# Kernel tuning notes

Measured on AMD Instinct MI355X. Metric: run time of the kernel, lower is better.

## Reference

```python
import jax, jax.numpy as jnp
import numpy as np

B, H, T, D = 2, 16, 2048, 64
BASE_WINDOW = 256
FULL = 999999


def _make_window_sizes(num_heads=H, base_window=BASE_WINDOW):
    ws = []
    for h in range(num_heads):
        if h < num_heads // 4:
            ws.append(base_window)
        elif h < num_heads // 2:
            ws.append(base_window * 2)
        elif h < 3 * num_heads // 4:
            ws.append(base_window * 4)
        else:
            ws.append(FULL)
    return jnp.asarray(ws, dtype=jnp.int32)


def setup_inputs() -> dict:
    key = jax.random.key(0)
    kq, kk, kv = jax.random.split(key, 3)
    Q = jax.random.normal(kq, (B, H, T, D), dtype=jnp.float32)
    K = jax.random.normal(kk, (B, H, T, D), dtype=jnp.float32)
    V = jax.random.normal(kv, (B, H, T, D), dtype=jnp.float32)
    return {"Q": Q, "K": K, "V": V, "window_sizes": _make_window_sizes()}


def reference(Q, K, V, window_sizes):
    b, h, t, d = Q.shape
    scale = 1.0 / np.sqrt(d).astype(np.float32)
    idx = jnp.arange(t, dtype=jnp.int32)
    diff = idx[:, None] - idx[None, :]  # [T, T], q_idx - kv_idx
    # causal & |q-k| <= w  ==  0 <= diff <= w  (per head)
    mask = (diff >= 0) & (diff[None, :, :] <= window_sizes[:, None, None])  # [H, T, T]
    scores = jnp.einsum('bhqd,bhkd->bhqk', Q, K) * scale  # [B, H, T, T]
    scores = jnp.where(mask[None], scores, -jnp.inf)
    attn = jax.nn.softmax(scores, axis=-1)
    return jnp.einsum('bhqk,bhkd->bhqd', attn, V)
```

## Files before the change

### kernel.cpp

```cpp
#include <hip/hip_runtime.h>


constexpr int Bc = 2, Hc = 16, Tc = 2048, Dc = 64;
constexpr int BQ = 64;
constexpr int BK = 64;
constexpr int KSTR = 72;
constexpr int VSTR = 72;
constexpr int PSTR = 72;
constexpr int N_ITEMS = Bc * Hc * (Tc / BQ);
constexpr float QSCALE = 0.125f * 1.44269504088896340736f;

constexpr int KOFF = 0;
constexpr int VOFF = 9216;
constexpr int POFF = 18432;
constexpr int IBOFF = 27648;

typedef __attribute__((ext_vector_type(8))) short short8;
typedef __attribute__((ext_vector_type(4))) float float4v;

__device__ inline unsigned f2bf_u(float f) {
    union { float f; unsigned u; } v; v.f = f;
    return (v.u + 0x7fffu + ((v.u >> 16) & 1u)) >> 16;
}

__device__ inline short8 pack8(const float* t) {
    short8 r;
#pragma unroll
    for (int j = 0; j < 8; j++) r[j] = (short)f2bf_u(t[j]);
    return r;
}

__global__ __launch_bounds__(512, 2)
void dswa_kernel(const float* __restrict__ Q, const float* __restrict__ K,
                 const float* __restrict__ V, const int* __restrict__ wsz,
                 float* __restrict__ O, unsigned* __restrict__ counter) {
    __shared__ __align__(16) unsigned short LDS[27648 + 8];

    const int tid  = threadIdx.x;
    const int g    = tid >> 8;
    const int ltid = tid & 255;
    const int wave = tid >> 6;
    const int wv   = wave & 3;
    const int lane = tid & 63;
    const int quad = lane >> 4;
    const int l16  = lane & 15;

    unsigned short* Kl = &LDS[KOFF + g * 4608];
    unsigned short* Vt = &LDS[VOFF + g * 4608];
    unsigned short* Pl = &LDS[POFF + wave * 1152];
    int* ib = (int*)&LDS[IBOFF];

    for (;;) {
        if (tid == 0) *ib = (int)atomicAdd(counter, 1u);
        __syncthreads();
        const int idx = *ib;
        if (idx >= N_ITEMS) break;

        const int b  = idx & 1;
        const int qt = 31 - ((idx >> 1) & 31);
        const int h  = 15 - (idx >> 6);
        const int q0 = qt * BQ;
        const int win = wsz[h];

        const size_t headoff = (size_t)(b * Hc + h) * Tc * Dc;
        const float* Qp = Q + headoff;
        const float* Kp = K + headoff;
        const float* Vp = V + headoff;
        float*       Op = O + headoff;

        short8 qf[2];
        {
            const int qrow = q0 + wv * 16 + l16;
#pragma unroll
            for (int c = 0; c < 2; c++) {
                const float* src = Qp + (size_t)qrow * Dc + c * 32 + quad * 8;
                float4v a = *(const float4v*)src;
                float4v d4 = *(const float4v*)(src + 4);
                float t[8] = {a[0]*QSCALE, a[1]*QSCALE, a[2]*QSCALE, a[3]*QSCALE,
                              d4[0]*QSCALE, d4[1]*QSCALE, d4[2]*QSCALE, d4[3]*QSCALE};
                qf[c] = pack8(t);
            }
        }

        float m_i = -1e30f, l_i = 0.0f;
        float4v acc[4];
#pragma unroll
        for (int nb = 0; nb < 4; nb++) acc[nb] = (float4v){0.f, 0.f, 0.f, 0.f};

        const int kv_lo = (max(0, q0 - win)) & ~(BK - 1);
        const int n_tiles = (q0 + BQ - kv_lo) >> 6;
        const int IT = (n_tiles + 1) >> 1;

        const int rg_rel0 = q0 + wv * 16 + l16 - quad * 4;

        for (int t = 0; t < IT; ++t) {
            const int ti = g + 2 * t;
            const bool act = ti < n_tiles;
            const int kv0 = kv_lo + ti * BK;

            __syncthreads();

            if (act) {
#pragma unroll
                for (int i = 0; i < 2; i++) {
                    const int key = (ltid >> 3) + 32 * i;
                    const int ds = (ltid & 7) * 8;
                    const float* src = Kp + (size_t)(kv0 + key) * Dc + ds;
                    float4v a = *(const float4v*)src;
                    float4v d4 = *(const float4v*)(src + 4);
                    float tt[8] = {a[0], a[1], a[2], a[3], d4[0], d4[1], d4[2], d4[3]};
                    *(short8*)&Kl[key * KSTR + ds] = pack8(tt);
                }
#pragma unroll
                for (int i = 0; i < 2; i++) {
                    const int d = ltid & 63;
                    const int kb = (ltid >> 6) * 8 + 32 * i;
                    float tt[8];
#pragma unroll
                    for (int j = 0; j < 8; j++) tt[j] = Vp[(size_t)(kv0 + kb + j) * Dc + d];
                    *(short8*)&Vt[d * VSTR + kb] = pack8(tt);
                }
            }
            __syncthreads();

            if (act) {
                float4v sT[4];
#pragma unroll
                for (int mb = 0; mb < 4; mb++) {
                    float4v c = {0.f, 0.f, 0.f, 0.f};
#pragma unroll
                    for (int ch = 0; ch < 2; ch++) {
                        short8 kf = *(short8*)&Kl[(mb * 16 + l16) * KSTR + ch * 32 + quad * 8];
                        c = __builtin_amdgcn_mfma_f32_16x16x32_bf16(kf, qf[ch], c, 0, 0, 0);
                    }
                    sT[mb] = c;
                }

                const int dbase = rg_rel0 - kv0;
#pragma unroll
                for (int mb = 0; mb < 4; mb++)
#pragma unroll
                    for (int r = 0; r < 4; r++) {
                        const unsigned diff = (unsigned)(dbase - mb * 16 - r);
                        sT[mb][r] = (diff <= (unsigned)win) ? sT[mb][r] : -3.0e38f;
                    }

                float mx = fmaxf(fmaxf(sT[0][0], sT[0][1]), fmaxf(sT[0][2], sT[0][3]));
#pragma unroll
                for (int mb = 1; mb < 4; mb++)
                    mx = fmaxf(mx, fmaxf(fmaxf(sT[mb][0], sT[mb][1]),
                                         fmaxf(sT[mb][2], sT[mb][3])));
                mx = fmaxf(mx, __shfl_xor(mx, 16));
                mx = fmaxf(mx, __shfl_xor(mx, 32));

                const float mn = fmaxf(m_i, mx);
                const float al = exp2f(m_i - mn);
                m_i = mn;

                float rs = 0.f;
                float p[4][4];
#pragma unroll
                for (int mb = 0; mb < 4; mb++)
#pragma unroll
                    for (int r = 0; r < 4; r++) {
                        p[mb][r] = exp2f(sT[mb][r] - mn);
                        rs += p[mb][r];
                    }
                rs += __shfl_xor(rs, 16);
                rs += __shfl_xor(rs, 32);
                l_i = l_i * al + rs;

#pragma unroll
                for (int mb = 0; mb < 4; mb++) {
                    unsigned u0 = f2bf_u(p[mb][0]) | (f2bf_u(p[mb][1]) << 16);
                    unsigned u1 = f2bf_u(p[mb][2]) | (f2bf_u(p[mb][3]) << 16);
                    unsigned* dst = (unsigned*)&Pl[l16 * PSTR + mb * 16 + quad * 4];
                    dst[0] = u0; dst[1] = u1;
                }

                float af[4];
#pragma unroll
                for (int r = 0; r < 4; r++) af[r] = __shfl(al, quad * 4 + r);
#pragma unroll
                for (int nb = 0; nb < 4; nb++)
#pragma unroll
                    for (int r = 0; r < 4; r++) acc[nb][r] *= af[r];

                __asm__ volatile("" ::: "memory");
                short8 pf[2];
#pragma unroll
                for (int ch = 0; ch < 2; ch++)
                    pf[ch] = *(short8*)&Pl[l16 * PSTR + ch * 32 + quad * 8];
#pragma unroll
                for (int nb = 0; nb < 4; nb++) {
#pragma unroll
                    for (int ch = 0; ch < 2; ch++) {
                        short8 vf = *(short8*)&Vt[(nb * 16 + l16) * VSTR + ch * 32 + quad * 8];
                        acc[nb] = __builtin_amdgcn_mfma_f32_16x16x32_bf16(pf[ch], vf, acc[nb], 0, 0, 0);
                    }
                }
            }
        }

        __syncthreads();
        float* fl = (float*)LDS;
        if (g == 1) {
            if (quad == 0) {
                fl[wv * 16 + l16] = m_i;
                fl[64 + wv * 16 + l16] = l_i;
            }
#pragma unroll
            for (int r = 0; r < 4; r++) {
                const int row = wv * 16 + quad * 4 + r;
#pragma unroll
                for (int nb = 0; nb < 4; nb++)
                    fl[128 + row * 65 + nb * 16 + l16] = acc[nb][r];
            }
        }
        __syncthreads();
        if (g == 0) {
            const float m1 = fl[wv * 16 + l16];
            const float l1 = fl[64 + wv * 16 + l16];
            const float M  = fmaxf(m_i, m1);
            const float a0 = exp2f(m_i - M);
            const float a1 = exp2f(m1 - M);
            const float lt = l_i * a0 + l1 * a1;
            const float inv = 1.0f / lt;
            float c0[4], c1[4], iv[4];
#pragma unroll
            for (int r = 0; r < 4; r++) {
                c0[r] = __shfl(a0, quad * 4 + r);
                c1[r] = __shfl(a1, quad * 4 + r);
                iv[r] = __shfl(inv, quad * 4 + r);
            }
#pragma unroll
            for (int r = 0; r < 4; r++) {
                const int row = wv * 16 + quad * 4 + r;
                float* dst = Op + (size_t)(q0 + row) * Dc;
#pragma unroll
                for (int nb = 0; nb < 4; nb++) {
                    const float o1 = fl[128 + row * 65 + nb * 16 + l16];
                    dst[nb * 16 + l16] = (acc[nb][r] * c0[r] + o1 * c1[r]) * iv[r];
                }
            }
        }
    }
}

extern "C" void kernel_launch(void* const* d_in, const int* in_sizes, int n_in,
                              void* d_out, int out_size, void* d_ws, size_t ws_size,
                              hipStream_t stream) {
    (void)in_sizes; (void)n_in; (void)ws_size; (void)out_size;
    const float* Q = (const float*)d_in[0];
    const float* K = (const float*)d_in[1];
    const float* V = (const float*)d_in[2];
    const int* wsz = (const int*)d_in[3];
    float* Out = (float*)d_out;
    unsigned* counter = (unsigned*)d_ws;

    hipMemsetAsync(counter, 0, sizeof(unsigned), stream);
    dim3 grid(512);
    dim3 block(512);
    dswa_kernel<<<grid, block, 0, stream>>>(Q, K, V, wsz, Out, counter);
}
```

Baseline: 140.8 us.

## Pre-convert K and transposed V to bf16 and prefetch next tile

Adds a pre-pass kernel that converts K to bf16 and V to a transposed bf16 layout in workspace, once per call. The attention kernel then loads ready-made short8 fragments instead of re-converting fp32 data and doing strided scalar V gathers for every tile. It also prefetches the next tile into registers after the barrier so the global loads overlap with compute. The cost is an extra kernel launch and extra global traffic for the bf16 copies. Launch bounds are raised to allow more blocks per CU.

```diff
diff --git a/kernel.cpp b/kernel.cpp
--- a/kernel.cpp
+++ b/kernel.cpp
@@ -10,6 +10,10 @@
 constexpr int N_ITEMS = Bc * Hc * (Tc / BQ);
 constexpr float QSCALE = 0.125f * 1.44269504088896340736f;
 
+constexpr size_t KB_OFF = 256;
+constexpr size_t VB_OFF = 256 + (size_t)Bc * Hc * Tc * Dc * 2;
+constexpr int HEADE = Tc * Dc;
+
 constexpr int KOFF = 0;
 constexpr int VOFF = 9216;
 constexpr int POFF = 18432;
@@ -30,9 +34,50 @@
     return r;
 }
 
-__global__ __launch_bounds__(512, 2)
-void dswa_kernel(const float* __restrict__ Q, const float* __restrict__ K,
-                 const float* __restrict__ V, const int* __restrict__ wsz,
+__global__ __launch_bounds__(256)
+void preconv_kernel(const float* __restrict__ K, const float* __restrict__ V,
+                    unsigned short* __restrict__ Kb, unsigned short* __restrict__ Vtb) {
+    const int blk = blockIdx.x;
+    const int tid = threadIdx.x;
+    if (blk < 2048) {
+        const int base = blk * 2048 + tid * 8;
+        float4v a = *(const float4v*)(K + base);
+        float4v b = *(const float4v*)(K + base + 4);
+        float t[8] = {a[0], a[1], a[2], a[3], b[0], b[1], b[2], b[3]};
+        *(short8*)(Kb + base) = pack8(t);
+    } else {
+        __shared__ float tile[64][65];
+        const int blk2 = blk - 2048;
+        const int bh = blk2 >> 5;
+        const int t0 = (blk2 & 31) * 64;
+        const float* src = V + (size_t)bh * HEADE + (size_t)t0 * Dc;
+#pragma unroll
+        for (int i = 0; i < 4; i++) {
+            const int r = (tid >> 4) + i * 16;
+            const int d4 = (tid & 15) * 4;
+            float4v v4 = *(const float4v*)(src + r * Dc + d4);
+            tile[r][d4] = v4[0]; tile[r][d4 + 1] = v4[1];
+            tile[r][d4 + 2] = v4[2]; tile[r][d4 + 3] = v4[3];
+        }
+        __syncthreads();
+        unsigned short* dst = Vtb + (size_t)bh * HEADE + t0;
+#pragma unroll
+        for (int i = 0; i < 2; i++) {
+            const int d = (tid >> 3) + 32 * i;
+            const int c = tid & 7;
+            float t[8];
+#pragma unroll
+            for (int j = 0; j < 8; j++) t[j] = tile[c * 8 + j][d];
+            *(short8*)(dst + (size_t)d * Tc + c * 8) = pack8(t);
+        }
+    }
+}
+
+__global__ __launch_bounds__(512, 4)
+void dswa_kernel(const float* __restrict__ Q,
+                 const unsigned short* __restrict__ Kb,
+                 const unsigned short* __restrict__ Vtb,
+                 const int* __restrict__ wsz,
                  float* __restrict__ O, unsigned* __restrict__ counter) {
     __shared__ __align__(16) unsigned short LDS[27648 + 8];
 
@@ -50,6 +95,9 @@
     unsigned short* Pl = &LDS[POFF + wave * 1152];
     int* ib = (int*)&LDS[IBOFF];
 
+    const int srow = ltid >> 3;
+    const int scol = (ltid & 7) * 8;
+
     for (;;) {
         if (tid == 0) *ib = (int)atomicAdd(counter, 1u);
         __syncthreads();
@@ -62,11 +110,11 @@
         const int q0 = qt * BQ;
         const int win = wsz[h];
 
-        const size_t headoff = (size_t)(b * Hc + h) * Tc * Dc;
+        const size_t headoff = (size_t)(b * Hc + h) * HEADE;
         const float* Qp = Q + headoff;
-        const float* Kp = K + headoff;
-        const float* Vp = V + headoff;
-        float*       Op = O + headoff;
+        const unsigned short* Kbh = Kb + headoff;
+        const unsigned short* Vbh = Vtb + headoff;
+        float* Op = O + headoff;
 
         short8 qf[2];
         {
@@ -93,6 +141,15 @@
 
         const int rg_rel0 = q0 + wv * 16 + l16 - quad * 4;
 
+        short8 kr0, kr1, vr0, vr1;
+        if (g < n_tiles) {
+            const int kv0 = kv_lo + g * BK;
+            kr0 = *(const short8*)(Kbh + (size_t)(kv0 + srow) * Dc + scol);
+            kr1 = *(const short8*)(Kbh + (size_t)(kv0 + srow + 32) * Dc + scol);
+            vr0 = *(const short8*)(Vbh + (size_t)srow * Tc + kv0 + scol);
+            vr1 = *(const short8*)(Vbh + (size_t)(srow + 32) * Tc + kv0 + scol);
+        }
+
         for (int t = 0; t < IT; ++t) {
             const int ti = g + 2 * t;
             const bool act = ti < n_tiles;
@@ -101,27 +158,21 @@
             __syncthreads();
 
             if (act) {
-#pragma unroll
-                for (int i = 0; i < 2; i++) {
-                    const int key = (ltid >> 3) + 32 * i;
-                    const int ds = (ltid & 7) * 8;
-                    const float* src = Kp + (size_t)(kv0 + key) * Dc + ds;
-                    float4v a = *(const float4v*)src;
-                    float4v d4 = *(const float4v*)(src + 4);
-                    float tt[8] = {a[0], a[1], a[2], a[3], d4[0], d4[1], d4[2], d4[3]};
-                    *(short8*)&Kl[key * KSTR + ds] = pack8(tt);
-                }
-#pragma unroll
-                for (int i = 0; i < 2; i++) {
-                    const int d = ltid & 63;
-                    const int kb = (ltid >> 6) * 8 + 32 * i;
-                    float tt[8];
-#pragma unroll
-                    for (int j = 0; j < 8; j++) tt[j] = Vp[(size_t)(kv0 + kb + j) * Dc + d];
-                    *(short8*)&Vt[d * VSTR + kb] = pack8(tt);
-                }
+                *(short8*)&Kl[srow * KSTR + scol] = kr0;
+                *(short8*)&Kl[(srow + 32) * KSTR + scol] = kr1;
+                *(short8*)&Vt[srow * VSTR + scol] = vr0;
+                *(short8*)&Vt[(srow + 32) * VSTR + scol] = vr1;
             }
             __syncthreads();
+
+            const int tn = ti + 2;
+            if (tn < n_tiles) {
+                const int kvn = kv_lo + tn * BK;
+                kr0 = *(const short8*)(Kbh + (size_t)(kvn + srow) * Dc + scol);
+                kr1 = *(const short8*)(Kbh + (size_t)(kvn + srow + 32) * Dc + scol);
+                vr0 = *(const short8*)(Vbh + (size_t)srow * Tc + kvn + scol);
+                vr1 = *(const short8*)(Vbh + (size_t)(srow + 32) * Tc + kvn + scol);
+            }
 
             if (act) {
                 float4v sT[4];
@@ -256,10 +307,12 @@
     const float* V = (const float*)d_in[2];
     const int* wsz = (const int*)d_in[3];
     float* Out = (float*)d_out;
+
     unsigned* counter = (unsigned*)d_ws;
+    unsigned short* Kb  = (unsigned short*)((char*)d_ws + KB_OFF);
+    unsigned short* Vtb = (unsigned short*)((char*)d_ws + VB_OFF);
 
     hipMemsetAsync(counter, 0, sizeof(unsigned), stream);
-    dim3 grid(512);
-    dim3 block(512);
-    dswa_kernel<<<grid, block, 0, stream>>>(Q, K, V, wsz, Out, counter);
-}
+    preconv_kernel<<<dim3(3072), dim3(256), 0, stream>>>(K, V, Kb, Vtb);
+    dswa_kernel<<<dim3(512), dim3(512), 0, stream>>>(Q, Kb, Vtb, wsz, Out, counter);
+}
```

Result: slower. 144.4 us (+2.6%).
